# Performance work log

Hardware: AMD Instinct MI355X
Metric: run time of the kernel (lower is better)

Reference implementation:

```python
import jax, jax.numpy as jnp
import numpy as np

B = 262144          # batch size
NUM_CLASSES = 1000  # number of classes in `classes` dict
CODE_LEN = 512      # length of each binary codeword in class_to_coding


def setup_inputs() -> dict:
    key = jax.random.key(0)
    k1, k2, k3 = jax.random.split(key, 3)
    output = jax.random.randint(k1, (B,), 0, NUM_CLASSES, dtype=jnp.int64 if jax.config.jax_enable_x64 else jnp.int32)
    target = jax.random.randint(k2, (B,), 0, NUM_CLASSES, dtype=output.dtype)
    # classes + class_to_coding fused into one [num_classes, code_len] binary table
    codebook = (jax.random.uniform(k3, (NUM_CLASSES, CODE_LEN)) > 0.5).astype(jnp.float32)
    return {"output": output, "target": target, "codebook": codebook}


def reference(output, target, codebook):
    # Vectorized equivalent of the per-sample Python loop:
    #   dist_i = sum(codebook[pred_i] != codebook[gt_i]); loss = mean_i dist_i
    pred_codes = codebook[output]   # [B, CODE_LEN]
    gt_codes = codebook[target]     # [B, CODE_LEN]
    dists = jnp.sum(pred_codes != gt_codes, axis=-1).astype(jnp.float32)  # [B]
    return jnp.mean(dists)
```

## Files before the change

kernel.cpp:

```cpp
#include <hip/hip_runtime.h>
#include <stdint.h>

#define B_SIZE        262144
#define NUM_CLASSES   1000
#define CODE_LEN      512
#define WORDS_PER_ROW 16
#define PACKED_WORDS  (NUM_CLASSES * WORDS_PER_ROW)
#define CHUNKS        (NUM_CLASSES * 4)
#define HAM_BLOCKS    128
#define SAMPLES_PER_BLOCK (B_SIZE / HAM_BLOCKS)

#define WS_DONE_OFF     0
#define WS_PART_OFF     128
#define WS_PART_STRIDE  32
#define WS_PACKED_OFF   32768

__global__ __launch_bounds__(256) void pack_kernel(
        const float* __restrict__ codebook,
        uint32_t* __restrict__ packed,
        unsigned int* __restrict__ done) {
    int tid = blockIdx.x * blockDim.x + threadIdx.x;
    if (tid == 0) *done = 0u;
    if (tid < NUM_CLASSES * CODE_LEN) {
        float x = codebook[tid];
        unsigned long long m = __ballot(x > 0.5f);
        if ((tid & 31) == 0) {
            packed[tid >> 5] = (uint32_t)(m >> (threadIdx.x & 32));
        }
    }
}

__global__ __launch_bounds__(256) void hamming_kernel(
        const int* __restrict__ output,
        const int* __restrict__ target,
        const uint32_t* __restrict__ packed,
        unsigned int* __restrict__ done,
        unsigned int* __restrict__ partials,
        float* __restrict__ out) {
    __shared__ uint4 lds[CHUNKS];
    __shared__ unsigned int wsum[4];
    __shared__ unsigned int last_flag;

    const uint4* pk4 = (const uint4*)packed;
    #pragma unroll
    for (int it = 0; it < 16; it++) {
        int g = threadIdx.x + 256 * it;
        if (g < CHUNKS) {
            int r = g >> 2, k = g & 3;
            lds[(r << 2) + ((k + (r >> 2)) & 3)] = pk4[g];
        }
    }
    __syncthreads();

    int base = blockIdx.x * SAMPLES_PER_BLOCK + threadIdx.x;
    unsigned int sum = 0;

    #pragma unroll
    for (int b = 0; b < 4; b++) {
        int i0 = base + b * 512;
        int i1 = i0 + 256;
        int o0 = output[i0], t0 = target[i0];
        int o1 = output[i1], t1 = target[i1];

        uint4 ao[4], at[4], bo[4], bt[4];
        int so0 = (o0 >> 2) & 3, st0 = (t0 >> 2) & 3;
        int so1 = (o1 >> 2) & 3, st1 = (t1 >> 2) & 3;
        #pragma unroll
        for (int k = 0; k < 4; k++) ao[k] = lds[(o0 << 2) + ((k + so0) & 3)];
        #pragma unroll
        for (int k = 0; k < 4; k++) at[k] = lds[(t0 << 2) + ((k + st0) & 3)];
        #pragma unroll
        for (int k = 0; k < 4; k++) bo[k] = lds[(o1 << 2) + ((k + so1) & 3)];
        #pragma unroll
        for (int k = 0; k < 4; k++) bt[k] = lds[(t1 << 2) + ((k + st1) & 3)];

        #pragma unroll
        for (int k = 0; k < 4; k++) {
            sum += __popc(ao[k].x ^ at[k].x) + __popc(ao[k].y ^ at[k].y)
                 + __popc(ao[k].z ^ at[k].z) + __popc(ao[k].w ^ at[k].w);
            sum += __popc(bo[k].x ^ bt[k].x) + __popc(bo[k].y ^ bt[k].y)
                 + __popc(bo[k].z ^ bt[k].z) + __popc(bo[k].w ^ bt[k].w);
        }
    }

    #pragma unroll
    for (int off = 32; off > 0; off >>= 1)
        sum += __shfl_down(sum, off, 64);
    if ((threadIdx.x & 63) == 0)
        wsum[threadIdx.x >> 6] = sum;
    __syncthreads();

    if (threadIdx.x == 0) {
        unsigned int bsum = wsum[0] + wsum[1] + wsum[2] + wsum[3];
        atomicExch(&partials[blockIdx.x * WS_PART_STRIDE], bsum);
        __threadfence();
        unsigned int prev = atomicAdd(done, 1u);
        last_flag = (prev == (unsigned int)(gridDim.x - 1)) ? 1u : 0u;
    }
    __syncthreads();

    if (last_flag) {
        unsigned int v = 0;
        if (threadIdx.x < HAM_BLOCKS)
            v = atomicAdd(&partials[threadIdx.x * WS_PART_STRIDE], 0u);
        #pragma unroll
        for (int off = 32; off > 0; off >>= 1)
            v += __shfl_down(v, off, 64);
        if ((threadIdx.x & 63) == 0)
            wsum[threadIdx.x >> 6] = v;
        __syncthreads();
        if (threadIdx.x == 0) {
            unsigned long long total = wsum[0] + wsum[1];
            out[0] = (float)((double)total / (double)B_SIZE);
        }
    }
}

extern "C" void kernel_launch(void* const* d_in, const int* in_sizes, int n_in,
                              void* d_out, int out_size, void* d_ws, size_t ws_size,
                              hipStream_t stream) {
    const int*   output   = (const int*)d_in[0];
    const int*   target   = (const int*)d_in[1];
    const float* codebook = (const float*)d_in[2];
    float* out = (float*)d_out;

    unsigned int* done     = (unsigned int*)((char*)d_ws + WS_DONE_OFF);
    unsigned int* partials = (unsigned int*)((char*)d_ws + WS_PART_OFF);
    uint32_t*     packed   = (uint32_t*)((char*)d_ws + WS_PACKED_OFF);

    pack_kernel<<<(NUM_CLASSES * CODE_LEN + 255) / 256, 256, 0, stream>>>(
        codebook, packed, done);
    hamming_kernel<<<HAM_BLOCKS, 256, 0, stream>>>(
        output, target, packed, done, partials, out);
}
```

Before: 66.09 us.

## Double hamming grid, prefetch indices before LDS fill, use separate finalize kernel

Doubles the number of hamming blocks so each block handles fewer samples, which spreads the work over more CUs. The output and target index loads are issued before the LDS codebook fill so their latency overlaps it. The last-block atomic counter and threadfence are replaced by a third single-block kernel that reduces the partials. That kernel adds one more launch, and every block still copies the full 64KB packed table into LDS.

```diff
diff --git a/kernel.cpp b/kernel.cpp
--- a/kernel.cpp
+++ b/kernel.cpp
@@ -4,23 +4,19 @@
 #define B_SIZE        262144
 #define NUM_CLASSES   1000
 #define CODE_LEN      512
-#define WORDS_PER_ROW 16
-#define PACKED_WORDS  (NUM_CLASSES * WORDS_PER_ROW)
+#define PACKED_WORDS  (NUM_CLASSES * 16)
 #define CHUNKS        (NUM_CLASSES * 4)
-#define HAM_BLOCKS    128
+#define HAM_BLOCKS    256
 #define SAMPLES_PER_BLOCK (B_SIZE / HAM_BLOCKS)
 
-#define WS_DONE_OFF     0
-#define WS_PART_OFF     128
+#define WS_PART_OFF     0
 #define WS_PART_STRIDE  32
-#define WS_PACKED_OFF   32768
+#define WS_PACKED_OFF   65536
 
 __global__ __launch_bounds__(256) void pack_kernel(
         const float* __restrict__ codebook,
-        uint32_t* __restrict__ packed,
-        unsigned int* __restrict__ done) {
+        uint32_t* __restrict__ packed) {
     int tid = blockIdx.x * blockDim.x + threadIdx.x;
-    if (tid == 0) *done = 0u;
     if (tid < NUM_CLASSES * CODE_LEN) {
         float x = codebook[tid];
         unsigned long long m = __ballot(x > 0.5f);
@@ -34,12 +30,17 @@
         const int* __restrict__ output,
         const int* __restrict__ target,
         const uint32_t* __restrict__ packed,
-        unsigned int* __restrict__ done,
-        unsigned int* __restrict__ partials,
-        float* __restrict__ out) {
+        unsigned int* __restrict__ partials) {
     __shared__ uint4 lds[CHUNKS];
     __shared__ unsigned int wsum[4];
-    __shared__ unsigned int last_flag;
+
+    int base = blockIdx.x * SAMPLES_PER_BLOCK + threadIdx.x;
+    int o[4], t[4];
+    #pragma unroll
+    for (int b = 0; b < 4; b++) {
+        o[b] = output[base + b * 256];
+        t[b] = target[base + b * 256];
+    }
 
     const uint4* pk4 = (const uint4*)packed;
     #pragma unroll
@@ -52,15 +53,11 @@
     }
     __syncthreads();
 
-    int base = blockIdx.x * SAMPLES_PER_BLOCK + threadIdx.x;
     unsigned int sum = 0;
-
     #pragma unroll
-    for (int b = 0; b < 4; b++) {
-        int i0 = base + b * 512;
-        int i1 = i0 + 256;
-        int o0 = output[i0], t0 = target[i0];
-        int o1 = output[i1], t1 = target[i1];
+    for (int b = 0; b < 2; b++) {
+        int o0 = o[2 * b], t0 = t[2 * b];
+        int o1 = o[2 * b + 1], t1 = t[2 * b + 1];
 
         uint4 ao[4], at[4], bo[4], bt[4];
         int so0 = (o0 >> 2) & 3, st0 = (t0 >> 2) & 3;
@@ -93,26 +90,24 @@
     if (threadIdx.x == 0) {
         unsigned int bsum = wsum[0] + wsum[1] + wsum[2] + wsum[3];
         atomicExch(&partials[blockIdx.x * WS_PART_STRIDE], bsum);
-        __threadfence();
-        unsigned int prev = atomicAdd(done, 1u);
-        last_flag = (prev == (unsigned int)(gridDim.x - 1)) ? 1u : 0u;
     }
+}
+
+__global__ __launch_bounds__(256) void finalize_kernel(
+        const unsigned int* __restrict__ partials,
+        float* __restrict__ out) {
+    __shared__ unsigned int wsum[4];
+    unsigned int v = partials[threadIdx.x * WS_PART_STRIDE];
+    #pragma unroll
+    for (int off = 32; off > 0; off >>= 1)
+        v += __shfl_down(v, off, 64);
+    if ((threadIdx.x & 63) == 0)
+        wsum[threadIdx.x >> 6] = v;
     __syncthreads();
-
-    if (last_flag) {
-        unsigned int v = 0;
-        if (threadIdx.x < HAM_BLOCKS)
-            v = atomicAdd(&partials[threadIdx.x * WS_PART_STRIDE], 0u);
-        #pragma unroll
-        for (int off = 32; off > 0; off >>= 1)
-            v += __shfl_down(v, off, 64);
-        if ((threadIdx.x & 63) == 0)
-            wsum[threadIdx.x >> 6] = v;
-        __syncthreads();
-        if (threadIdx.x == 0) {
-            unsigned long long total = wsum[0] + wsum[1];
-            out[0] = (float)((double)total / (double)B_SIZE);
-        }
+    if (threadIdx.x == 0) {
+        unsigned long long total =
+            (unsigned long long)wsum[0] + wsum[1] + wsum[2] + wsum[3];
+        out[0] = (float)((double)total / (double)B_SIZE);
     }
 }
 
@@ -124,12 +119,12 @@
     const float* codebook = (const float*)d_in[2];
     float* out = (float*)d_out;
 
-    unsigned int* done     = (unsigned int*)((char*)d_ws + WS_DONE_OFF);
     unsigned int* partials = (unsigned int*)((char*)d_ws + WS_PART_OFF);
     uint32_t*     packed   = (uint32_t*)((char*)d_ws + WS_PACKED_OFF);
 
     pack_kernel<<<(NUM_CLASSES * CODE_LEN + 255) / 256, 256, 0, stream>>>(
-        codebook, packed, done);
+        codebook, packed);
     hamming_kernel<<<HAM_BLOCKS, 256, 0, stream>>>(
-        output, target, packed, done, partials, out);
+        output, target, packed, partials);
+    finalize_kernel<<<1, 256, 0, stream>>>(partials, out);
 }
```

After: 63.95 us. -3.2%, faster.
